# Kernel tuning notes

Measured on AMD Instinct MI355X. Metric: run time of the kernel, lower is better.

## Reference

```python
import jax, jax.numpy as jnp
import numpy as np

B, N, C, K = 32, 1024, 14, 9      # graphs, residues/graph, atom channels, kNN
E, H, NC = 128, 128, 25           # embed_size, hidden_size, num_classes
NG = 128                          # gaussians in time embedding (== embed_size)


def _ffn(x, W1, b1, W2, b2):
    # nn.Sequential(SiLU, Linear, SiLU, Linear)
    h = jax.nn.silu(x) @ W1 + b1
    return jax.nn.silu(h) @ W2 + b2


def _time_emb(t, Wt1, bt1, Wt2, bt2):
    # GaussianSmearing(0,1,NG) -> Linear -> ReLU -> Linear
    offset = jnp.linspace(0.0, 1.0, NG)
    coeff = -0.5 / (offset[1] - offset[0]) ** 2
    d = t[..., None] - offset + 1e-6
    g = jnp.exp(coeff * d * d)
    return jax.nn.relu(g @ Wt1 + bt1) @ Wt2 + bt2


def _forward(S, X, t, emb, Wt1, bt1, Wt2, bt2, We1, be1, We2, be2,
             Wx1, bx1, Wx2, bx2, Wh1, bh1, Wh2, bh2,
             Wd1, bd1, Wd2, bd2, Wp1, bp1, Wr1, br1, Wr2, br2):
    H0 = emb[S]                                           # [B,N,E]
    Hh = H0 + _time_emb(t, Wt1, bt1, Wt2, bt2)            # H_0 + time_emb
    # dynamic kNN graph on CA coordinates (channel 1), per graph
    ca = X[:, :, 1]                                       # [B,N,3]
    d2 = jnp.sum((ca[:, :, None] - ca[:, None]) ** 2, -1) # [B,N,N]
    d2 = d2 + jnp.eye(N, dtype=d2.dtype) * 1e10           # no self loops
    _, idx = jax.lax.top_k(-d2, K)                        # [B,N,K] neighbor ids
    gather = jax.vmap(lambda a, i: a[i])                  # per-graph gather
    Xnb = gather(X, idx)                                  # [B,N,K,C,3]
    Hnb = gather(Hh, idx)                                 # [B,N,K,E]
    rel = X[:, :, None] - Xnb                             # [B,N,K,C,3]
    # multi-channel radial features (EGNN-style channel Gram matrix)
    radial = jnp.einsum('bnkcd,bnked->bnkce', rel, rel).reshape(B, N, K, C * C) / C
    Hi = jnp.broadcast_to(Hh[:, :, None], (B, N, K, E))
    m = _ffn(jnp.concatenate([Hi, Hnb, radial], -1), We1, be1, We2, be2)  # [B,N,K,H]
    # EGNN coordinate update
    w = _ffn(m, Wx1, bx1, Wx2, bx2)                       # [B,N,K,1]
    X_out = X + jnp.mean(rel * w[..., None], axis=2)      # [B,N,C,3]
    # node update
    Hn = Hh + _ffn(jnp.concatenate([Hh, jnp.sum(m, 2)], -1), Wh1, bh1, Wh2, bh2)
    # symmetric edge-distance FFN: f([src,dst]) + f([dst,src])
    Hs = jnp.broadcast_to(Hn[:, :, None], (B, N, K, E))
    Hd = gather(Hn, idx)
    pd = (_ffn(jnp.concatenate([Hs, Hd], -1), Wd1, bd1, Wd2, bd2)
          + _ffn(jnp.concatenate([Hd, Hs], -1), Wd1, bd1, Wd2, bd2))[..., 0]  # [B,N,K]
    # pred_logits = ffn_residue2(pre_H_0 * sigmoid(ffn_proj(H)))
    gate = jax.nn.sigmoid(jax.nn.silu(Hn) @ Wp1 + bp1)
    logits = _ffn(H0 * gate, Wr1, br1, Wr2, br2)          # [B,N,NC]
    return logits, X_out, pd


def setup_inputs() -> dict:
    key = jax.random.key(0)
    ks = jax.random.split(key, 34)
    p = lambda k, s: (0.02 * jax.random.normal(k, s)).astype(jnp.float32)
    inp = {
        'X': jax.random.normal(ks[0], (B, N, C, 3), jnp.float32),
        'S': jax.random.randint(ks[1], (B, N), 0, NC),
        't': jax.random.uniform(ks[2], (B, N), jnp.float32),
        'emb': p(ks[3], (NC, E)),
        'Wt1': p(ks[4], (NG, H)), 'bt1': jnp.zeros((H,), jnp.float32),
        'Wt2': p(ks[5], (H, E)), 'bt2': jnp.zeros((E,), jnp.float32),
        'We1': p(ks[6], (2 * E + C * C, H)), 'be1': jnp.zeros((H,), jnp.float32),
        'We2': p(ks[7], (H, H)), 'be2': jnp.zeros((H,), jnp.float32),
        'Wx1': p(ks[8], (H, H)), 'bx1': jnp.zeros((H,), jnp.float32),
        'Wx2': p(ks[9], (H, 1)), 'bx2': jnp.zeros((1,), jnp.float32),
        'Wh1': p(ks[10], (E + H, H)), 'bh1': jnp.zeros((H,), jnp.float32),
        'Wh2': p(ks[11], (H, E)), 'bh2': jnp.zeros((E,), jnp.float32),
        'Wd1': p(ks[12], (2 * E, H)), 'bd1': jnp.zeros((H,), jnp.float32),
        'Wd2': p(ks[13], (H, 1)), 'bd2': jnp.zeros((1,), jnp.float32),
        'Wp1': p(ks[14], (E, E)), 'bp1': jnp.zeros((E,), jnp.float32),
        'Wr1': p(ks[15], (E, H)), 'br1': jnp.zeros((H,), jnp.float32),
        'Wr2': p(ks[16], (H, NC)), 'br2': jnp.zeros((NC,), jnp.float32),
    }
    return inp


def reference(X, S, t, emb, Wt1, bt1, Wt2, bt2, We1, be1, We2, be2,
              Wx1, bx1, Wx2, bx2, Wh1, bh1, Wh2, bh2,
              Wd1, bd1, Wd2, bd2, Wp1, bp1, Wr1, br1, Wr2, br2):
    return _forward(S, X, t, emb, Wt1, bt1, Wt2, bt2, We1, be1, We2, be2,
                    Wx1, bx1, Wx2, bx2, Wh1, bh1, Wh2, bh2,
                    Wd1, bd1, Wd2, bd2, Wp1, bp1, Wr1, br1, Wr2, br2)
```

## Files before the change

### kernel.cpp

```cpp
#include <hip/hip_runtime.h>

#define BATCH 32
#define NPT   1024
#define CC    14
#define KNN   9
#define EDIM  128
#define HDIM  128
#define NCLS  25
#define BN    (BATCH*NPT)

#define RSTR  236
#define SSTR  140

typedef float  v4f __attribute__((ext_vector_type(4)));
typedef __bf16 v8bf __attribute__((ext_vector_type(8)));

__device__ __forceinline__ float silu_f(float x) {
    const float e = __expf(-x);
    return x * __builtin_amdgcn_rcpf(1.0f + e);
}
__device__ __forceinline__ float sigm_f(float x) {
    const float e = __expf(-x);
    return __builtin_amdgcn_rcpf(1.0f + e);
}
// ... 34 lines not shown
    i -= 16384;
    if (i < 32768) { const int c = i/256, k = i%256; Wh1t[i] = f2bf_rne(Wh1[(size_t)k*128 + c]); return; }
    i -= 32768;
    if (i < 16384) { Wh2t[i] = f2bf_rne(Wh2[(size_t)(i % 128)*128 + i/128]); return; }
    i -= 16384;
    if (i < 32768) {
        const int t = i/128, k = i%128;
        Wd1t[i] = f2bf_rne((t < 128) ? Wd1[(size_t)k*128 + t] : Wd1[(size_t)(128 + k)*128 + (t - 128)]);
        return;
    }
    i -= 32768;
    if (i < 16384) { Wp1t[i] = f2bf_rne(Wp1[(size_t)(i % 128)*128 + i/128]); return; }
    i -= 16384;
    if (i < 16384) { Wr1t[i] = f2bf_rne(Wr1[(size_t)(i % 128)*128 + i/128]); return; }
    i -= 16384;
    if (i < 16384) { Wt1t[i] = f2bf_rne(Wt1[(size_t)(i % 128)*128 + i/128]); return; }
    i -= 16384;
    if (i < 16384) { Wt2t[i] = f2bf_rne(Wt2[(size_t)(i % 128)*128 + i/128]); return; }
    i -= 16384;
    if (i < 32768) {
        const int t = i/128, k = i%128;
        We1Ft[i] = f2bf_rne((t < 128) ? We1[(size_t)k*128 + t] : We1[(size_t)(128 + k)*128 + (t - 128)]);
    }
}

__global__ __launch_bounds__(256) void k_hhP(
    const float* __restrict__ t, const int* __restrict__ S,
    const float* __restrict__ emb,
    const unsigned short* __restrict__ Wt1t, const float* __restrict__ bt1,
    const unsigned short* __restrict__ Wt2t, const float* __restrict__ bt2,
    const unsigned short* __restrict__ We1Ft, const float* __restrict__ be1,
    float* __restrict__ Hh, float* __restrict__ P)
{
    __shared__ __align__(16) unsigned short A0[16*140];
    __shared__ __align__(16) unsigned short A1[16*140];
    __shared__ __align__(16) unsigned short A2[16*140];
    __shared__ int sInt[16];

    const int tid  = threadIdx.x;
    const int wv   = tid >> 6, lane = tid & 63;
    const int quad = lane >> 4, r16 = lane & 15;
    const int col  = tid & 127, rh = tid >> 7;
    const int base = blockIdx.x * 16;

    if (tid < 16) sInt[tid] = S[base + tid];

    const float step  = 1.0f / 127.0f;
    const float coeff = -0.5f / (step * step);
    const float off   = step * (float)col;
    #pragma unroll
    for (int rr = 0; rr < 8; ++rr) {
        const int r = rh*8 + rr;
        const float d = t[base + r] - off + 1e-6f;
        A0[r*140 + col] = f2bf(__expf(coeff * d * d));
    }
    __syncthreads();

    {
        v8bf a[4];
        #pragma unroll
        for (int ks = 0; ks < 4; ++ks)
            a[ks] = *(const v8bf*)(A0 + r16*140 + ks*32 + quad*8);
        #pragma unroll
        for (int c2 = 0; c2 < 2; ++c2) {
            const int ch = (wv*2 + c2)*16 + r16;
            v4f acc = (v4f){0,0,0,0};
            #pragma unroll
            for (int ks = 0; ks < 4; ++ks) {
                const v8bf bb = *(const v8bf*)(Wt1t + (size_t)ch*128 + ks*32 + quad*8);
                acc = __builtin_amdgcn_mfma_f32_16x16x32_bf16(a[ks], bb, acc, 0, 0, 0);
            }
            const float bc = bt1[ch];
            #pragma unroll
            for (int rr = 0; rr < 4; ++rr)
                A1[(quad*4 + rr)*140 + ch] = f2bf(fmaxf(acc[rr] + bc, 0.0f));
        }
    }
    __syncthreads();

    {
        v8bf a[4];
        #pragma unroll
        for (int ks = 0; ks < 4; ++ks)
            a[ks] = *(const v8bf*)(A1 + r16*140 + ks*32 + quad*8);
        #pragma unroll
        for (int c2 = 0; c2 < 2; ++c2) {
            const int ch = (wv*2 + c2)*16 + r16;
            v4f acc = (v4f){0,0,0,0};
            #pragma unroll
            for (int ks = 0; ks < 4; ++ks) {
                const v8bf bb = *(const v8bf*)(Wt2t + (size_t)ch*128 + ks*32 + quad*8);
                acc = __builtin_amdgcn_mfma_f32_16x16x32_bf16(a[ks], bb, acc, 0, 0, 0);
            }
            const float bc = bt2[ch];
            #pragma unroll
            for (int rr = 0; rr < 4; ++rr) {
                const int row = quad*4 + rr;
                const int node = base + row;
                const float hh = emb[sInt[row]*128 + ch] + acc[rr] + bc;
                Hh[(size_t)node*128 + ch] = hh;
                A2[row*140 + ch] = f2bf(silu_f(hh));
            }
        }
    }
    __syncthreads();

    {
        v8bf a[4];
        #pragma unroll
        for (int ks = 0; ks < 4; ++ks)
            a[ks] = *(const v8bf*)(A2 + r16*140 + ks*32 + quad*8);
        #pragma unroll
        for (int c2 = 0; c2 < 4; ++c2) {
            const int ch = (wv*4 + c2)*16 + r16;
            v4f acc = (v4f){0,0,0,0};
            #pragma unroll
            for (int ks = 0; ks < 4; ++ks) {
                const v8bf bb = *(const v8bf*)(We1Ft + (size_t)ch*128 + ks*32 + quad*8);
                acc = __builtin_amdgcn_mfma_f32_16x16x32_bf16(a[ks], bb, acc, 0, 0, 0);
            }
            const float fb = (ch < 128) ? be1[ch] : 0.0f;
            #pragma unroll
            for (int rr = 0; rr < 4; ++rr)
                P[(size_t)(base + quad*4 + rr)*256 + ch] = acc[rr] + fb;
        }
    }
}

__global__ __launch_bounds__(256) void k_knn(
    const float* __restrict__ X, int* __restrict__ idxb)
{
    __shared__ __align__(16) float4 Cc[NPT];
    __shared__ float dsh[4][64][KNN];
    __shared__ int   ish[4][64][KNN];

    const int tid = threadIdx.x, lane = tid & 63, wv = tid >> 6;
    const int bb = blockIdx.x >> 4;
    const int n0 = (blockIdx.x & 15) << 6;
    const float* Xb = X + (size_t)bb * NPT * 42;

    for (int i = tid; i < NPT; i += 256) {
        const float* p = Xb + (size_t)i*42 + 3;
        Cc[i] = make_float4(p[0], p[1], p[2], 0.0f);
    }
    __syncthreads();

    const int n = n0 + lane;
    const float4 c = Cc[n];

    float dist[KNN]; int ind[KNN];
    #pragma unroll
    for (int k = 0; k < KNN; ++k) { dist[k] = 3.0e38f; ind[k] = -1; }

    const int j0 = wv * 256;
    for (int jj = 0; jj < 256; ++jj) {
        const int j = j0 + jj;
        const float4 q = Cc[j];
// ... 24 lines not shown
        for (int w = 0; w < 4; ++w)
            #pragma unroll
            for (int k = 0; k < KNN; ++k) {
                const float d = dsh[w][tid][k];
                const int   i = ish[w][tid][k];
                if (d < fd[KNN-1]) {
                    fd[KNN-1] = d; fi[KNN-1] = i;
                    #pragma unroll
                    for (int p = KNN-1; p > 0; --p) {
                        if (fd[p] < fd[p-1]) {
                            float td = fd[p]; fd[p] = fd[p-1]; fd[p-1] = td;
                            int   ti = fi[p]; fi[p] = fi[p-1]; fi[p-1] = ti;
                        }
                    }
                }
            }
        const int node = (bb << 10) + n0 + tid;
        #pragma unroll
        for (int k = 0; k < KNN; ++k) idxb[(size_t)node*KNN + k] = fi[k];
    }
}

__global__ __launch_bounds__(256) void k_edge(
    const float* __restrict__ X, const int* __restrict__ idxb,
    const float* __restrict__ P,
    const unsigned short* __restrict__ WeRt,
    const unsigned short* __restrict__ We2t,
    const unsigned short* __restrict__ Wx1t,
    const float* __restrict__ be2,
    const float* __restrict__ bx1, const float* __restrict__ Wx2,
    const float* __restrict__ bx2,
    float* __restrict__ msum, float* __restrict__ wbuf)
{
    __shared__ unsigned short radF[16*RSTR];
    __shared__ unsigned short silA[16*SSTR];
    __shared__ unsigned short silB[16*SSTR];
    __shared__ __align__(16) float relS[16][57];
    __shared__ __align__(16) float xS[16][57];
    __shared__ float wred[KNN][16][4];
    __shared__ int   jsh[16][12];

    const int tid  = threadIdx.x;
    const int wv   = tid >> 6, lane = tid & 63;
    const int quad = lane >> 4, r16 = lane & 15;
    const int node0 = blockIdx.x * 16;
    const int b     = node0 >> 10;
    const int chan0 = (wv*2 + 0)*16 + r16;
    const int chan1 = (wv*2 + 1)*16 + r16;
    const int srow  = tid >> 4, c16 = tid & 15;

    if (tid < 144) jsh[tid/9][tid%9] = idxb[(size_t)(node0 + tid/9)*KNN + tid%9];
    {
        const int i0 = c16*3;
        if (i0 < 42) {
            #pragma unroll
            for (int k = 0; k < 3; ++k)
                xS[srow][c16*4 + k] = X[(size_t)(node0 + srow)*42 + i0 + k];
        }
    }

    float pn0[4], pn1[4];
    #pragma unroll
    for (int rr = 0; rr < 4; ++rr) {
        pn0[rr] = P[(size_t)(node0 + quad*4 + rr)*256 + chan0];
        pn1[rr] = P[(size_t)(node0 + quad*4 + rr)*256 + chan1];
    }
    const float be2c0 = be2[chan0], be2c1 = be2[chan1];
    const float bxc0  = bx1[chan0], bxc1  = bx1[chan1];
    const float wxc0  = Wx2[chan0], wxc1  = Wx2[chan1];

    v8bf B1[2][7], B2[2][4], B3[2][4];
    #pragma unroll
    for (int c2 = 0; c2 < 2; ++c2) {
        const int ct = wv*2 + c2;
        #pragma unroll
        for (int ks = 0; ks < 7; ++ks)
            B1[c2][ks] = *(const v8bf*)(WeRt + (size_t)(ct*16 + r16)*224 + ks*32 + quad*8);
        #pragma unroll
        for (int ks = 0; ks < 4; ++ks) {
            B2[c2][ks] = *(const v8bf*)(We2t + (size_t)(ct*16 + r16)*128 + ks*32 + quad*8);
            B3[c2][ks] = *(const v8bf*)(Wx1t + (size_t)(ct*16 + r16)*128 + ks*32 + quad*8);
        }
    }

    float msA0[4] = {0,0,0,0}, msA1[4] = {0,0,0,0};

    __syncthreads();

    for (int t = 0; t < KNN; ++t) {
        {
            const int j  = jsh[srow][t];
            const int i0 = c16*3;
            if (i0 < 42) {
                const size_t jb = (size_t)((b << 10) + j)*42;
                #pragma unroll
                for (int k = 0; k < 3; ++k)
                    relS[srow][c16*4 + k] = xS[srow][c16*4 + k] - X[jb + i0 + k];
            }
        }
        __syncthreads();

        {
            const float* rb = relS[srow];
            #pragma unroll
            for (int kk = 0; kk < 14; ++kk) {
                const int f = c16 + 16*kk;
                if (f < 196) {
                    const int cI = f / 14, eI = f % 14;
                    const float v = (rb[cI*4]*rb[eI*4] + rb[cI*4+1]*rb[eI*4+1]
                                   + rb[cI*4+2]*rb[eI*4+2]) * (1.0f/14.0f);
                    radF[srow*RSTR + f] = f2bf(silu_f(v));
                } else {
                    radF[srow*RSTR + f] = 0;
                }
            }
        }
        __syncthreads();

        v4f acc10 = (v4f){0,0,0,0}, acc11 = (v4f){0,0,0,0};
        #pragma unroll
        for (int ks = 0; ks < 7; ++ks) {
            const v8bf a = *(const v8bf*)(radF + r16*RSTR + ks*32 + quad*8);
            acc10 = __builtin_amdgcn_mfma_f32_16x16x32_bf16(a, B1[0][ks], acc10, 0, 0, 0);
            acc11 = __builtin_amdgcn_mfma_f32_16x16x32_bf16(a, B1[1][ks], acc11, 0, 0, 0);
        }
        {
            float pj0[4], pj1[4];
            #pragma unroll
            for (int rr = 0; rr < 4; ++rr) {
                const int jq = jsh[quad*4 + rr][t];
                const size_t jrow = (size_t)((b << 10) + jq)*256 + 128;
                pj0[rr] = P[jrow + chan0];
                pj1[rr] = P[jrow + chan1];
            }
            #pragma unroll
            for (int rr = 0; rr < 4; ++rr) {
                const int rw = quad*4 + rr;
                silA[rw*SSTR + chan0] = f2bf(silu_f(acc10[rr] + pn0[rr] + pj0[rr]));
                silA[rw*SSTR + chan1] = f2bf(silu_f(acc11[rr] + pn1[rr] + pj1[rr]));
            }
        }
        __syncthreads();

        v4f acc20 = (v4f){0,0,0,0}, acc21 = (v4f){0,0,0,0};
        #pragma unroll
        for (int ks = 0; ks < 4; ++ks) {
            const v8bf a = *(const v8bf*)(silA + r16*SSTR + ks*32 + quad*8);
            acc20 = __builtin_amdgcn_mfma_f32_16x16x32_bf16(a, B2[0][ks], acc20, 0, 0, 0);
            acc21 = __builtin_amdgcn_mfma_f32_16x16x32_bf16(a, B2[1][ks], acc21, 0, 0, 0);
        }
        #pragma unroll
        for (int rr = 0; rr < 4; ++rr) {
            const float m0 = acc20[rr] + be2c0;
            const float m1 = acc21[rr] + be2c1;
            msA0[rr] += m0;  msA1[rr] += m1;
            const int rw = quad*4 + rr;
            silB[rw*SSTR + chan0] = f2bf(silu_f(m0));
            silB[rw*SSTR + chan1] = f2bf(silu_f(m1));
        }
        __syncthreads();

        v4f acc30 = (v4f){0,0,0,0}, acc31 = (v4f){0,0,0,0};
        #pragma unroll
        for (int ks = 0; ks < 4; ++ks) {
            const v8bf a = *(const v8bf*)(silB + r16*SSTR + ks*32 + quad*8);
            acc30 = __builtin_amdgcn_mfma_f32_16x16x32_bf16(a, B3[0][ks], acc30, 0, 0, 0);
            acc31 = __builtin_amdgcn_mfma_f32_16x16x32_bf16(a, B3[1][ks], acc31, 0, 0, 0);
        }
        #pragma unroll
        for (int rr = 0; rr < 4; ++rr) {
            float pr = silu_f(acc30[rr] + bxc0) * wxc0
                     + silu_f(acc31[rr] + bxc1) * wxc1;
            pr += __shfl_xor(pr, 1);
            pr += __shfl_xor(pr, 2);
            pr += __shfl_xor(pr, 4);
            pr += __shfl_xor(pr, 8);
            if (r16 == 0) wred[t][quad*4 + rr][wv] = pr;
        }
    }

    #pragma unroll
    for (int rr = 0; rr < 4; ++rr) {
        msum[(size_t)(node0 + quad*4 + rr)*128 + chan0] = msA0[rr];
        msum[(size_t)(node0 + quad*4 + rr)*128 + chan1] = msA1[rr];
    }
    __syncthreads();
    if (tid < 16*KNN) {
        const int tt = tid / 16, rw = tid % 16;
        wbuf[(size_t)(node0 + rw)*KNN + tt] =
            wred[tt][rw][0] + wred[tt][rw][1] + wred[tt][rw][2] + wred[tt][rw][3] + bx2[0];
    }
}

__global__ __launch_bounds__(256) void k_nodeF(
    const float* __restrict__ X, const float* __restrict__ Hh,
    const float* __restrict__ msum, const int* __restrict__ idxb,
    const float* __restrict__ wbuf,
    const unsigned short* __restrict__ Wh1t, const float* __restrict__ bh1,
    const unsigned short* __restrict__ Wh2t, const float* __restrict__ bh2,
    const unsigned short* __restrict__ Wd1t, const float* __restrict__ bd1,
    const int* __restrict__ S, const float* __restrict__ emb,
    const unsigned short* __restrict__ Wp1t, const float* __restrict__ bp1,
    const unsigned short* __restrict__ Wr1t, const float* __restrict__ br1,
    const float* __restrict__ Wr2, const float* __restrict__ br2,
    float* __restrict__ Hn, float* __restrict__ AB,
    float* __restrict__ outL, float* __restrict__ outX)
{
    __shared__ __align__(16) unsigned short A0[16*268];
    __shared__ __align__(16) unsigned short A1[16*140];
    __shared__ __align__(16) unsigned short A2[16*140];
    __shared__ __align__(16) unsigned short A3[16*140];
    __shared__ int sInt[16];
    float* A4 = (float*)A0;

    const int tid  = threadIdx.x;
    const int wv   = tid >> 6, lane = tid & 63;
    const int quad = lane >> 4, r16 = lane & 15;
    const int base = blockIdx.x * 16;

    if (tid < 16) sInt[tid] = S[base + tid];
    for (int r = 0; r < 16; ++r) {
        const int node = base + r;
        const float v = (tid < 128) ? Hh[(size_t)node*128 + tid]
                                    : msum[(size_t)node*128 + (tid - 128)];
        A0[r*268 + tid] = f2bf(silu_f(v));
    }
    __syncthreads();

    {
        v8bf a[8];
        #pragma unroll
        for (int ks = 0; ks < 8; ++ks)
            a[ks] = *(const v8bf*)(A0 + r16*268 + ks*32 + quad*8);
        #pragma unroll
        for (int c2 = 0; c2 < 2; ++c2) {
            const int ch = (wv*2 + c2)*16 + r16;
            v4f acc = (v4f){0,0,0,0};
            #pragma unroll
            for (int ks = 0; ks < 8; ++ks) {
                const v8bf bb = *(const v8bf*)(Wh1t + (size_t)ch*256 + ks*32 + quad*8);
                acc = __builtin_amdgcn_mfma_f32_16x16x32_bf16(a[ks], bb, acc, 0, 0, 0);
            }
            const float bc = bh1[ch];
            #pragma unroll
            for (int rr = 0; rr < 4; ++rr)
                A1[(quad*4 + rr)*140 + ch] = f2bf(silu_f(acc[rr] + bc));
        }
    }
    __syncthreads();

    {
        v8bf a[4];
        #pragma unroll
        for (int ks = 0; ks < 4; ++ks)
            a[ks] = *(const v8bf*)(A1 + r16*140 + ks*32 + quad*8);
        #pragma unroll
        for (int c2 = 0; c2 < 2; ++c2) {
            const int ch = (wv*2 + c2)*16 + r16;
            v4f acc = (v4f){0,0,0,0};
            #pragma unroll
            for (int ks = 0; ks < 4; ++ks) {
                const v8bf bb = *(const v8bf*)(Wh2t + (size_t)ch*128 + ks*32 + quad*8);
                acc = __builtin_amdgcn_mfma_f32_16x16x32_bf16(a[ks], bb, acc, 0, 0, 0);
            }
            const float bc = bh2[ch];
            #pragma unroll
            for (int rr = 0; rr < 4; ++rr) {
                const int row = quad*4 + rr;
                const int node = base + row;
                const float hn = Hh[(size_t)node*128 + ch] + acc[rr] + bc;
                Hn[(size_t)node*128 + ch] = hn;
                A2[row*140 + ch] = f2bf(silu_f(hn));
            }
        }
    }
    __syncthreads();

    {
        v8bf a[4];
        #pragma unroll
        for (int ks = 0; ks < 4; ++ks)
            a[ks] = *(const v8bf*)(A2 + r16*140 + ks*32 + quad*8);

        #pragma unroll
        for (int cg = 0; cg < 2; ++cg) {
            #pragma unroll
            for (int c2 = 0; c2 < 2; ++c2) {
                const int ch = (wv*4 + cg*2 + c2)*16 + r16;
                v4f acc = (v4f){0,0,0,0};
                #pragma unroll
                for (int ks = 0; ks < 4; ++ks) {
                    const v8bf bb = *(const v8bf*)(Wd1t + (size_t)ch*128 + ks*32 + quad*8);
                    acc = __builtin_amdgcn_mfma_f32_16x16x32_bf16(a[ks], bb, acc, 0, 0, 0);
                }
                const float fb = (ch < 128) ? bd1[ch] : 0.0f;
                #pragma unroll
                for (int rr = 0; rr < 4; ++rr)
                    AB[(size_t)(base + quad*4 + rr)*256 + ch] = acc[rr] + fb;
            }
        }

        #pragma unroll
        for (int c2 = 0; c2 < 2; ++c2) {
            const int ch = (wv*2 + c2)*16 + r16;
            v4f acc = (v4f){0,0,0,0};
            #pragma unroll
            for (int ks = 0; ks < 4; ++ks) {
                const v8bf bb = *(const v8bf*)(Wp1t + (size_t)ch*128 + ks*32 + quad*8);
                acc = __builtin_amdgcn_mfma_f32_16x16x32_bf16(a[ks], bb, acc, 0, 0, 0);
            }
            const float bc = bp1[ch];
            #pragma unroll
            for (int rr = 0; rr < 4; ++rr) {
                const int row = quad*4 + rr;
                const float g = sigm_f(acc[rr] + bc);
                const float x = emb[sInt[row]*128 + ch] * g;
                A3[row*140 + ch] = f2bf(silu_f(x));
            }
        }
    }
    __syncthreads();

    {
        v8bf a[4];
        #pragma unroll
        for (int ks = 0; ks < 4; ++ks)
            a[ks] = *(const v8bf*)(A3 + r16*140 + ks*32 + quad*8);
        #pragma unroll
        for (int c2 = 0; c2 < 2; ++c2) {
            const int ch = (wv*2 + c2)*16 + r16;
            v4f acc = (v4f){0,0,0,0};
            #pragma unroll
            for (int ks = 0; ks < 4; ++ks) {
                const v8bf bb = *(const v8bf*)(Wr1t + (size_t)ch*128 + ks*32 + quad*8);
                acc = __builtin_amdgcn_mfma_f32_16x16x32_bf16(a[ks], bb, acc, 0, 0, 0);
            }
            const float bc = br1[ch];
            #pragma unroll
            for (int rr = 0; rr < 4; ++rr)
                A4[(quad*4 + rr)*134 + ch] = silu_f(acc[rr] + bc);
        }
    }
    __syncthreads();

    for (int o = tid; o < 16*NCLS; o += 256) {
        const int r = o / NCLS, j = o % NCLS;
        float s = 0.0f;
        for (int i = 0; i < 128; ++i) s += A4[r*134 + i] * Wr2[i*NCLS + j];
        outL[(size_t)(base + r)*NCLS + j] = s + br2[j];
    }

    for (int o = tid; o < 16*CC*3; o += 256) {
        const int r = o / (CC*3), q = o % (CC*3);
        const int node = base + r;
        const int bq = node >> 10;
        const int cq = q / 3, dc = q % 3;
        const float xv = X[((size_t)node*CC + cq)*3 + dc];
        float a = 0.0f;
        for (int k = 0; k < KNN; ++k) {
            const int j = idxb[(size_t)node*KNN + k];
            const float xj = X[(((size_t)(bq << 10) + j)*CC + cq)*3 + dc];
            a += (xv - xj) * wbuf[(size_t)node*KNN + k];
        }
        outX[(size_t)node*CC*3 + q] = xv + a / 9.0f;
    }
}

__global__ __launch_bounds__(256) void k_pd2(
    const float* __restrict__ AB, const int* __restrict__ idxb,
    const float* __restrict__ Wd2, const float* __restrict__ bd2,
    float* __restrict__ outPd)
{
    const int tid  = threadIdx.x;
    const int lane = tid & 63, wv = tid >> 6;
    const int c0   = lane, c1 = lane + 64;
    const float w0 = Wd2[c0], w1 = Wd2[c1];
    const float b2 = 2.0f * bd2[0];

    #pragma unroll
    for (int s = 0; s < 2; ++s) {
        const int node = blockIdx.x * 8 + wv*2 + s;
        const int b    = node >> 10;

        int jv = 0;
        if (lane < KNN) jv = idxb[(size_t)node*KNN + lane];

        const float An0 = AB[(size_t)node*256 + c0];
        const float An1 = AB[(size_t)node*256 + c1];
        const float Bn0 = AB[(size_t)node*256 + 128 + c0];
        const float Bn1 = AB[(size_t)node*256 + 128 + c1];

        float Aj0[KNN], Aj1[KNN], Bj0[KNN], Bj1[KNN];
        #pragma unroll
        for (int e = 0; e < KNN; ++e) {
            const size_t jn = (size_t)((b << 10) + __shfl(jv, e)) * 256;
// ... 42 lines not shown
    const float* Wp1 = (const float*)d_in[24];
    const float* bp1 = (const float*)d_in[25];
    const float* Wr1 = (const float*)d_in[26];
    const float* br1 = (const float*)d_in[27];
    const float* Wr2 = (const float*)d_in[28];
    const float* br2 = (const float*)d_in[29];

    float* out   = (float*)d_out;
    float* outL  = out;
    float* outX  = out + (size_t)BN*NCLS;
    float* outPd = outX + (size_t)BN*CC*3;

    unsigned short* WeRt  = (unsigned short*)d_ws;
    unsigned short* We2t  = WeRt  + 28672;
    unsigned short* Wx1t  = We2t  + 16384;
    unsigned short* Wh1t  = Wx1t  + 16384;
    unsigned short* Wh2t  = Wh1t  + 32768;
    unsigned short* Wd1t  = Wh2t  + 16384;
    unsigned short* Wp1t  = Wd1t  + 32768;
    unsigned short* Wr1t  = Wp1t  + 16384;
    unsigned short* Wt1t  = Wr1t  + 16384;
    unsigned short* Wt2t  = Wt1t  + 16384;
    unsigned short* We1Ft = Wt2t  + 16384;
    float* Hh   = (float*)(We1Ft + 32768);
    float* msum = Hh   + (size_t)BN*EDIM;
    float* Hn   = msum + (size_t)BN*HDIM;
    float* wbuf = Hn   + (size_t)BN*EDIM;
    float* P    = wbuf + (size_t)BN*KNN;
    int*   idxb = (int*)(P + (size_t)BN*256);

    k_prep  <<<944,    256, 0, stream>>>(We1, We2, Wx1, Wh1, Wh2, Wd1, Wp1, Wr1, Wt1, Wt2,
                                         WeRt, We2t, Wx1t, Wh1t, Wh2t, Wd1t, Wp1t, Wr1t,
                                         Wt1t, Wt2t, We1Ft);
    k_hhP   <<<BN/16,  256, 0, stream>>>(t, S, emb, Wt1t, bt1, Wt2t, bt2, We1Ft, be1, Hh, P);
    k_knn   <<<BN/64,  256, 0, stream>>>(X, idxb);
    k_edge  <<<BN/16,  256, 0, stream>>>(X, idxb, P, WeRt, We2t, Wx1t,
                                         be2, bx1, Wx2, bx2, msum, wbuf);
    k_nodeF <<<BN/16,  256, 0, stream>>>(X, Hh, msum, idxb, wbuf,
                                         Wh1t, bh1, Wh2t, bh2, Wd1t, bd1,
                                         S, emb, Wp1t, bp1, Wr1t, br1, Wr2, br2,
                                         Hn, P, outL, outX);
    k_pd2   <<<BN/8,   256, 0, stream>>>(P, idxb, Wd2, bd2, outPd);
}
```

Baseline: 503.9 us.

## Process 32 nodes per block so each weight fragment feeds two MFMA row groups

```diff
diff --git a/kernel.cpp b/kernel.cpp
--- a/kernel.cpp
+++ b/kernel.cpp
@@ -90,97 +90,112 @@
     const unsigned short* __restrict__ We1Ft, const float* __restrict__ be1,
     float* __restrict__ Hh, float* __restrict__ P)
 {
-    __shared__ __align__(16) unsigned short A0[16*140];
-    __shared__ __align__(16) unsigned short A1[16*140];
-    __shared__ __align__(16) unsigned short A2[16*140];
-    __shared__ int sInt[16];
+    __shared__ __align__(16) unsigned short A0[32*140];
+    __shared__ __align__(16) unsigned short A1[32*140];
+    __shared__ __align__(16) unsigned short A2[32*140];
+    __shared__ int sInt[32];
 
     const int tid  = threadIdx.x;
     const int wv   = tid >> 6, lane = tid & 63;
     const int quad = lane >> 4, r16 = lane & 15;
     const int col  = tid & 127, rh = tid >> 7;
-    const int base = blockIdx.x * 16;
-
-    if (tid < 16) sInt[tid] = S[base + tid];
+    const int base = blockIdx.x * 32;
+
+    if (tid < 32) sInt[tid] = S[base + tid];
 
     const float step  = 1.0f / 127.0f;
     const float coeff = -0.5f / (step * step);
     const float off   = step * (float)col;
     #pragma unroll
-    for (int rr = 0; rr < 8; ++rr) {
-        const int r = rh*8 + rr;
+    for (int rr = 0; rr < 16; ++rr) {
+        const int r = rh*16 + rr;
         const float d = t[base + r] - off + 1e-6f;
         A0[r*140 + col] = f2bf(__expf(coeff * d * d));
     }
     __syncthreads();
 
     {
-        v8bf a[4];
-        #pragma unroll
-        for (int ks = 0; ks < 4; ++ks)
-            a[ks] = *(const v8bf*)(A0 + r16*140 + ks*32 + quad*8);
+        v8bf a[2][4];
+        #pragma unroll
+        for (int g = 0; g < 2; ++g)
+            #pragma unroll
+            for (int ks = 0; ks < 4; ++ks)
+                a[g][ks] = *(const v8bf*)(A0 + (16*g + r16)*140 + ks*32 + quad*8);
         #pragma unroll
         for (int c2 = 0; c2 < 2; ++c2) {
             const int ch = (wv*2 + c2)*16 + r16;
-            v4f acc = (v4f){0,0,0,0};
+            v4f acc[2] = {(v4f){0,0,0,0}, (v4f){0,0,0,0}};
             #pragma unroll
             for (int ks = 0; ks < 4; ++ks) {
                 const v8bf bb = *(const v8bf*)(Wt1t + (size_t)ch*128 + ks*32 + quad*8);
-                acc = __builtin_amdgcn_mfma_f32_16x16x32_bf16(a[ks], bb, acc, 0, 0, 0);
+                acc[0] = __builtin_amdgcn_mfma_f32_16x16x32_bf16(a[0][ks], bb, acc[0], 0, 0, 0);
+                acc[1] = __builtin_amdgcn_mfma_f32_16x16x32_bf16(a[1][ks], bb, acc[1], 0, 0, 0);
             }
             const float bc = bt1[ch];
             #pragma unroll
-            for (int rr = 0; rr < 4; ++rr)
-                A1[(quad*4 + rr)*140 + ch] = f2bf(fmaxf(acc[rr] + bc, 0.0f));
+            for (int g = 0; g < 2; ++g)
+                #pragma unroll
+                for (int rr = 0; rr < 4; ++rr)
+                    A1[(16*g + quad*4 + rr)*140 + ch] = f2bf(fmaxf(acc[g][rr] + bc, 0.0f));
         }
     }
     __syncthreads();
 
     {
-        v8bf a[4];
-        #pragma unroll
-        for (int ks = 0; ks < 4; ++ks)
-            a[ks] = *(const v8bf*)(A1 + r16*140 + ks*32 + quad*8);
+        v8bf a[2][4];
+        #pragma unroll
+        for (int g = 0; g < 2; ++g)
+            #pragma unroll
+            for (int ks = 0; ks < 4; ++ks)
+                a[g][ks] = *(const v8bf*)(A1 + (16*g + r16)*140 + ks*32 + quad*8);
         #pragma unroll
         for (int c2 = 0; c2 < 2; ++c2) {
             const int ch = (wv*2 + c2)*16 + r16;
-            v4f acc = (v4f){0,0,0,0};
+            v4f acc[2] = {(v4f){0,0,0,0}, (v4f){0,0,0,0}};
             #pragma unroll
             for (int ks = 0; ks < 4; ++ks) {
                 const v8bf bb = *(const v8bf*)(Wt2t + (size_t)ch*128 + ks*32 + quad*8);
-                acc = __builtin_amdgcn_mfma_f32_16x16x32_bf16(a[ks], bb, acc, 0, 0, 0);
+                acc[0] = __builtin_amdgcn_mfma_f32_16x16x32_bf16(a[0][ks], bb, acc[0], 0, 0, 0);
+                acc[1] = __builtin_amdgcn_mfma_f32_16x16x32_bf16(a[1][ks], bb, acc[1], 0, 0, 0);
             }
             const float bc = bt2[ch];
             #pragma unroll
-            for (int rr = 0; rr < 4; ++rr) {
-                const int row = quad*4 + rr;
-                const int node = base + row;
-                const float hh = emb[sInt[row]*128 + ch] + acc[rr] + bc;
-                Hh[(size_t)node*128 + ch] = hh;
-                A2[row*140 + ch] = f2bf(silu_f(hh));
-            }
+            for (int g = 0; g < 2; ++g)
+                #pragma unroll
+                for (int rr = 0; rr < 4; ++rr) {
+                    const int row = 16*g + quad*4 + rr;
+                    const int node = base + row;
+                    const float hh = emb[sInt[row]*128 + ch] + acc[g][rr] + bc;
+                    Hh[(size_t)node*128 + ch] = hh;
+                    A2[row*140 + ch] = f2bf(silu_f(hh));
+                }
         }
     }
     __syncthreads();
 
     {
-        v8bf a[4];
-        #pragma unroll
-        for (int ks = 0; ks < 4; ++ks)
-            a[ks] = *(const v8bf*)(A2 + r16*140 + ks*32 + quad*8);
+        v8bf a[2][4];
+        #pragma unroll
+        for (int g = 0; g < 2; ++g)
+            #pragma unroll
+            for (int ks = 0; ks < 4; ++ks)
+                a[g][ks] = *(const v8bf*)(A2 + (16*g + r16)*140 + ks*32 + quad*8);
         #pragma unroll
         for (int c2 = 0; c2 < 4; ++c2) {
             const int ch = (wv*4 + c2)*16 + r16;
-            v4f acc = (v4f){0,0,0,0};
+            v4f acc[2] = {(v4f){0,0,0,0}, (v4f){0,0,0,0}};
             #pragma unroll
             for (int ks = 0; ks < 4; ++ks) {
                 const v8bf bb = *(const v8bf*)(We1Ft + (size_t)ch*128 + ks*32 + quad*8);
-                acc = __builtin_amdgcn_mfma_f32_16x16x32_bf16(a[ks], bb, acc, 0, 0, 0);
+                acc[0] = __builtin_amdgcn_mfma_f32_16x16x32_bf16(a[0][ks], bb, acc[0], 0, 0, 0);
+                acc[1] = __builtin_amdgcn_mfma_f32_16x16x32_bf16(a[1][ks], bb, acc[1], 0, 0, 0);
             }
             const float fb = (ch < 128) ? be1[ch] : 0.0f;
             #pragma unroll
-            for (int rr = 0; rr < 4; ++rr)
-                P[(size_t)(base + quad*4 + rr)*256 + ch] = acc[rr] + fb;
+            for (int g = 0; g < 2; ++g)
+                #pragma unroll
+                for (int rr = 0; rr < 4; ++rr)
+                    P[(size_t)(base + 16*g + quad*4 + rr)*256 + ch] = acc[g][rr] + fb;
         }
     }
 }
@@ -271,76 +286,103 @@
     const float* __restrict__ bx2,
     float* __restrict__ msum, float* __restrict__ wbuf)
 {
-    __shared__ unsigned short radF[16*RSTR];
-    __shared__ unsigned short silA[16*SSTR];
-    __shared__ unsigned short silB[16*SSTR];
-    __shared__ __align__(16) float relS[16][57];
-    __shared__ __align__(16) float xS[16][57];
-    __shared__ float wred[KNN][16][4];
-    __shared__ int   jsh[16][12];
+    __shared__ unsigned short radF[32*RSTR];
+    __shared__ __align__(16) unsigned char UA[32*SSTR*2];
+    __shared__ unsigned short silB[32*SSTR];
+    __shared__ float wred[KNN][32][4];
+    __shared__ int   jsh[32][KNN];
+
+    unsigned short* silA = (unsigned short*)UA;
+    float*          relS = (float*)UA;
 
     const int tid  = threadIdx.x;
     const int wv   = tid >> 6, lane = tid & 63;
     const int quad = lane >> 4, r16 = lane & 15;
-    const int node0 = blockIdx.x * 16;
+    const int node0 = blockIdx.x * 32;
     const int b     = node0 >> 10;
     const int chan0 = (wv*2 + 0)*16 + r16;
     const int chan1 = (wv*2 + 1)*16 + r16;
     const int srow  = tid >> 4, c16 = tid & 15;
 
-    if (tid < 144) jsh[tid/9][tid%9] = idxb[(size_t)(node0 + tid/9)*KNN + tid%9];
-    {
-        const int i0 = c16*3;
-        if (i0 < 42) {
+    for (int o = tid; o < 32*KNN; o += 256)
+        jsh[o/KNN][o%KNN] = idxb[(size_t)(node0 + o/KNN)*KNN + o%KNN];
+
+    float xr[2][3] = {{0,0,0},{0,0,0}};
+    if (c16 < 14) {
+        #pragma unroll
+        for (int g = 0; g < 2; ++g)
             #pragma unroll
             for (int k = 0; k < 3; ++k)
-                xS[srow][c16*4 + k] = X[(size_t)(node0 + srow)*42 + i0 + k];
-        }
-    }
-
-    float pn0[4], pn1[4];
+                xr[g][k] = X[(size_t)(node0 + srow + 16*g)*42 + c16*3 + k];
+    }
+
+    float pn0[2][4], pn1[2][4];
     #pragma unroll
-    for (int rr = 0; rr < 4; ++rr) {
-        pn0[rr] = P[(size_t)(node0 + quad*4 + rr)*256 + chan0];
-        pn1[rr] = P[(size_t)(node0 + quad*4 + rr)*256 + chan1];
-    }
+    for (int g = 0; g < 2; ++g)
+        #pragma unroll
+        for (int rr = 0; rr < 4; ++rr) {
+            const size_t nrow = (size_t)(node0 + 16*g + quad*4 + rr)*256;
+            pn0[g][rr] = P[nrow + chan0];
+            pn1[g][rr] = P[nrow + chan1];
+        }
     const float be2c0 = be2[chan0], be2c1 = be2[chan1];
     const float bxc0  = bx1[chan0], bxc1  = bx1[chan1];
     const float wxc0  = Wx2[chan0], wxc1  = Wx2[chan1];
 
-    v8bf B1[2][7], B2[2][4], B3[2][4];
-    #pragma unroll
-    for (int c2 = 0; c2 < 2; ++c2) {
-        const int ct = wv*2 + c2;
-        #pragma unroll
-        for (int ks = 0; ks < 7; ++ks)
-            B1[c2][ks] = *(const v8bf*)(WeRt + (size_t)(ct*16 + r16)*224 + ks*32 + quad*8);
-        #pragma unroll
-        for (int ks = 0; ks < 4; ++ks) {
-            B2[c2][ks] = *(const v8bf*)(We2t + (size_t)(ct*16 + r16)*128 + ks*32 + quad*8);
-            B3[c2][ks] = *(const v8bf*)(Wx1t + (size_t)(ct*16 + r16)*128 + ks*32 + quad*8);
-        }
-    }
-
-    float msA0[4] = {0,0,0,0}, msA1[4] = {0,0,0,0};
-
-    __syncthreads();
+    float msA0[2][4] = {{0,0,0,0},{0,0,0,0}};
+    float msA1[2][4] = {{0,0,0,0},{0,0,0,0}};
+
+    __syncthreads();
+
+    float xj[2][3];
+    if (c16 < 14) {
+        #pragma unroll
+        for (int g = 0; g < 2; ++g) {
+            const int j = jsh[srow + 16*g][0];
+            #pragma unroll
+            for (int k = 0; k < 3; ++k)
+                xj[g][k] = X[(size_t)((b << 10) + j)*42 + c16*3 + k];
+        }
+    }
 
     for (int t = 0; t < KNN; ++t) {
-        {
-            const int j  = jsh[srow][t];
-            const int i0 = c16*3;
-            if (i0 < 42) {
-                const size_t jb = (size_t)((b << 10) + j)*42;
+        if (c16 < 14) {
+            #pragma unroll
+            for (int g = 0; g < 2; ++g)
                 #pragma unroll
                 for (int k = 0; k < 3; ++k)
-                    relS[srow][c16*4 + k] = xS[srow][c16*4 + k] - X[jb + i0 + k];
-            }
-        }
-        __syncthreads();
-
-        {
-            const float* rb = relS[srow];
+                    relS[(srow + 16*g)*70 + c16*4 + k] = xr[g][k] - xj[g][k];
+        }
+        if (t + 1 < KNN && c16 < 14) {
+            #pragma unroll
+            for (int g = 0; g < 2; ++g) {
+                const int j = jsh[srow + 16*g][t+1];
+                #pragma unroll
+                for (int k = 0; k < 3; ++k)
+                    xj[g][k] = X[(size_t)((b << 10) + j)*42 + c16*3 + k];
+            }
+        }
+        float pj0[2][4], pj1[2][4];
+        #pragma unroll
+        for (int g = 0; g < 2; ++g)
+            #pragma unroll
+            for (int rr = 0; rr < 4; ++rr) {
+                const int jq = jsh[16*g + quad*4 + rr][t];
+                const size_t jrow = (size_t)((b << 10) + jq)*256 + 128;
+                pj0[g][rr] = P[jrow + chan0];
+                pj1[g][rr] = P[jrow + chan1];
+            }
+        v8bf B1c0[7], B1c1[7];
+        #pragma unroll
+        for (int ks = 0; ks < 7; ++ks) {
+            B1c0[ks] = *(const v8bf*)(WeRt + (size_t)chan0*224 + ks*32 + quad*8);
+            B1c1[ks] = *(const v8bf*)(WeRt + (size_t)chan1*224 + ks*32 + quad*8);
+        }
+
+        #pragma unroll
+        for (int g = 0; g < 2; ++g) {
+            const int row = srow + 16*g;
+            const float* rb = relS + row*70;
             #pragma unroll
             for (int kk = 0; kk < 14; ++kk) {
                 const int f = c16 + 16*kk;
@@ -348,84 +390,103 @@
                     const int cI = f / 14, eI = f % 14;
                     const float v = (rb[cI*4]*rb[eI*4] + rb[cI*4+1]*rb[eI*4+1]
                                    + rb[cI*4+2]*rb[eI*4+2]) * (1.0f/14.0f);
-                    radF[srow*RSTR + f] = f2bf(silu_f(v));
+                    radF[row*RSTR + f] = f2bf(silu_f(v));
                 } else {
-                    radF[srow*RSTR + f] = 0;
+                    radF[row*RSTR + f] = 0;
                 }
             }
         }
         __syncthreads();
 
-        v4f acc10 = (v4f){0,0,0,0}, acc11 = (v4f){0,0,0,0};
-        #pragma unroll
-        for (int ks = 0; ks < 7; ++ks) {
-            const v8bf a = *(const v8bf*)(radF + r16*RSTR + ks*32 + quad*8);
-            acc10 = __builtin_amdgcn_mfma_f32_16x16x32_bf16(a, B1[0][ks], acc10, 0, 0, 0);
-            acc11 = __builtin_amdgcn_mfma_f32_16x16x32_bf16(a, B1[1][ks], acc11, 0, 0, 0);
-        }
-        {
-            float pj0[4], pj1[4];
+        v4f a10[2] = {(v4f){0,0,0,0},(v4f){0,0,0,0}};
+        v4f a11[2] = {(v4f){0,0,0,0},(v4f){0,0,0,0}};
+        #pragma unroll
+        for (int g = 0; g < 2; ++g)
+            #pragma unroll
+            for (int ks = 0; ks < 7; ++ks) {
+                const v8bf a = *(const v8bf*)(radF + (16*g + r16)*RSTR + ks*32 + quad*8);
+                a10[g] = __builtin_amdgcn_mfma_f32_16x16x32_bf16(a, B1c0[ks], a10[g], 0, 0, 0);
+                a11[g] = __builtin_amdgcn_mfma_f32_16x16x32_bf16(a, B1c1[ks], a11[g], 0, 0, 0);
+            }
+        v8bf B2c0[4], B2c1[4];
+        #pragma unroll
+        for (int ks = 0; ks < 4; ++ks) {
+            B2c0[ks] = *(const v8bf*)(We2t + (size_t)chan0*128 + ks*32 + quad*8);
+            B2c1[ks] = *(const v8bf*)(We2t + (size_t)chan1*128 + ks*32 + quad*8);
+        }
+        #pragma unroll
+        for (int g = 0; g < 2; ++g)
             #pragma unroll
             for (int rr = 0; rr < 4; ++rr) {
-                const int jq = jsh[quad*4 + rr][t];
-                const size_t jrow = (size_t)((b << 10) + jq)*256 + 128;
-                pj0[rr] = P[jrow + chan0];
-                pj1[rr] = P[jrow + chan1];
-            }
+                const int rw = 16*g + quad*4 + rr;
+                silA[rw*SSTR + chan0] = f2bf(silu_f(a10[g][rr] + pn0[g][rr] + pj0[g][rr]));
+                silA[rw*SSTR + chan1] = f2bf(silu_f(a11[g][rr] + pn1[g][rr] + pj1[g][rr]));
+            }
+        __syncthreads();
+
+        v4f a20[2] = {(v4f){0,0,0,0},(v4f){0,0,0,0}};
+        v4f a21[2] = {(v4f){0,0,0,0},(v4f){0,0,0,0}};
+        #pragma unroll
+        for (int g = 0; g < 2; ++g)
+            #pragma unroll
+            for (int ks = 0; ks < 4; ++ks) {
+                const v8bf a = *(const v8bf*)(silA + (16*g + r16)*SSTR + ks*32 + quad*8);
+                a20[g] = __builtin_amdgcn_mfma_f32_16x16x32_bf16(a, B2c0[ks], a20[g], 0, 0, 0);
+                a21[g] = __builtin_amdgcn_mfma_f32_16x16x32_bf16(a, B2c1[ks], a21[g], 0, 0, 0);
+            }
+        v8bf B3c0[4], B3c1[4];
+        #pragma unroll
+        for (int ks = 0; ks < 4; ++ks) {
+            B3c0[ks] = *(const v8bf*)(Wx1t + (size_t)chan0*128 + ks*32 + quad*8);
+            B3c1[ks] = *(const v8bf*)(Wx1t + (size_t)chan1*128 + ks*32 + quad*8);
+        }
+        #pragma unroll
+        for (int g = 0; g < 2; ++g)
             #pragma unroll
             for (int rr = 0; rr < 4; ++rr) {
-                const int rw = quad*4 + rr;
-                silA[rw*SSTR + chan0] = f2bf(silu_f(acc10[rr] + pn0[rr] + pj0[rr]));
-                silA[rw*SSTR + chan1] = f2bf(silu_f(acc11[rr] + pn1[rr] + pj1[rr]));
-            }
-        }
+                const float m0 = a20[g][rr] + be2c0;
+                const float m1 = a21[g][rr] + be2c1;
+                msA0[g][rr] += m0;  msA1[g][rr] += m1;
+                const int rw = 16*g + quad*4 + rr;
+                silB[rw*SSTR + chan0] = f2bf(silu_f(m0));
+                silB[rw*SSTR + chan1] = f2bf(silu_f(m1));
+            }
         __syncthreads();
 
-        v4f acc20 = (v4f){0,0,0,0}, acc21 = (v4f){0,0,0,0};
-        #pragma unroll
-        for (int ks = 0; ks < 4; ++ks) {
-            const v8bf a = *(const v8bf*)(silA + r16*SSTR + ks*32 + quad*8);
-            acc20 = __builtin_amdgcn_mfma_f32_16x16x32_bf16(a, B2[0][ks], acc20, 0, 0, 0);
-            acc21 = __builtin_amdgcn_mfma_f32_16x16x32_bf16(a, B2[1][ks], acc21, 0, 0, 0);
-        }
+        v4f a30[2] = {(v4f){0,0,0,0},(v4f){0,0,0,0}};
+        v4f a31[2] = {(v4f){0,0,0,0},(v4f){0,0,0,0}};
+        #pragma unroll
+        for (int g = 0; g < 2; ++g)
+            #pragma unroll
+            for (int ks = 0; ks < 4; ++ks) {
+                const v8bf a = *(const v8bf*)(silB + (16*g + r16)*SSTR + ks*32 + quad*8);
+                a30[g] = __builtin_amdgcn_mfma_f32_16x16x32_bf16(a, B3c0[ks], a30[g], 0, 0, 0);
+                a31[g] = __builtin_amdgcn_mfma_f32_16x16x32_bf16(a, B3c1[ks], a31[g], 0, 0, 0);
+            }
+        #pragma unroll
+        for (int g = 0; g < 2; ++g)
+            #pragma unroll
+            for (int rr = 0; rr < 4; ++rr) {
+                float pr = silu_f(a30[g][rr] + bxc0) * wxc0
+                         + silu_f(a31[g][rr] + bxc1) * wxc1;
+                pr += __shfl_xor(pr, 1);
+                pr += __shfl_xor(pr, 2);
+                pr += __shfl_xor(pr, 4);
+                pr += __shfl_xor(pr, 8);
+                if (r16 == 0) wred[t][16*g + quad*4 + rr][wv] = pr;
+            }
+    }
+
+    #pragma unroll
+    for (int g = 0; g < 2; ++g)
         #pragma unroll
         for (int rr = 0; rr < 4; ++rr) {
-            const float m0 = acc20[rr] + be2c0;
-            const float m1 = acc21[rr] + be2c1;
-            msA0[rr] += m0;  msA1[rr] += m1;
-            const int rw = quad*4 + rr;
-            silB[rw*SSTR + chan0] = f2bf(silu_f(m0));
-            silB[rw*SSTR + chan1] = f2bf(silu_f(m1));
-        }
-        __syncthreads();
-
-        v4f acc30 = (v4f){0,0,0,0}, acc31 = (v4f){0,0,0,0};
-        #pragma unroll
-        for (int ks = 0; ks < 4; ++ks) {
-            const v8bf a = *(const v8bf*)(silB + r16*SSTR + ks*32 + quad*8);
-            acc30 = __builtin_amdgcn_mfma_f32_16x16x32_bf16(a, B3[0][ks], acc30, 0, 0, 0);
-            acc31 = __builtin_amdgcn_mfma_f32_16x16x32_bf16(a, B3[1][ks], acc31, 0, 0, 0);
-        }
-        #pragma unroll
-        for (int rr = 0; rr < 4; ++rr) {
-            float pr = silu_f(acc30[rr] + bxc0) * wxc0
-                     + silu_f(acc31[rr] + bxc1) * wxc1;
-            pr += __shfl_xor(pr, 1);
-            pr += __shfl_xor(pr, 2);
-            pr += __shfl_xor(pr, 4);
-            pr += __shfl_xor(pr, 8);
-            if (r16 == 0) wred[t][quad*4 + rr][wv] = pr;
-        }
-    }
-
-    #pragma unroll
-    for (int rr = 0; rr < 4; ++rr) {
-        msum[(size_t)(node0 + quad*4 + rr)*128 + chan0] = msA0[rr];
-        msum[(size_t)(node0 + quad*4 + rr)*128 + chan1] = msA1[rr];
-    }
-    __syncthreads();
-    if (tid < 16*KNN) {
-        const int tt = tid / 16, rw = tid % 16;
+            msum[(size_t)(node0 + 16*g + quad*4 + rr)*128 + chan0] = msA0[g][rr];
+            msum[(size_t)(node0 + 16*g + quad*4 + rr)*128 + chan1] = msA1[g][rr];
+        }
+    __syncthreads();
+    for (int o = tid; o < 32*KNN; o += 256) {
+        const int tt = o / 32, rw = o % 32;
         wbuf[(size_t)(node0 + rw)*KNN + tt] =
             wred[tt][rw][0] + wred[tt][rw][1] + wred[tt][rw][2] + wred[tt][rw][3] + bx2[0];
     }
@@ -445,20 +506,20 @@
     float* __restrict__ Hn, float* __restrict__ AB,
     float* __restrict__ outL, float* __restrict__ outX)
 {
-    __shared__ __align__(16) unsigned short A0[16*268];
-    __shared__ __align__(16) unsigned short A1[16*140];
-    __shared__ __align__(16) unsigned short A2[16*140];
-    __shared__ __align__(16) unsigned short A3[16*140];
-    __shared__ int sInt[16];
+    __shared__ __align__(16) unsigned short A0[32*268];
+    __shared__ __align__(16) unsigned short A1[32*140];
+    __shared__ __align__(16) unsigned short A2[32*140];
+    __shared__ __align__(16) unsigned short A3[32*140];
+    __shared__ int sInt[32];
     float* A4 = (float*)A0;
 
     const int tid  = threadIdx.x;
     const int wv   = tid >> 6, lane = tid & 63;
     const int quad = lane >> 4, r16 = lane & 15;
-    const int base = blockIdx.x * 16;
-
-    if (tid < 16) sInt[tid] = S[base + tid];
-    for (int r = 0; r < 16; ++r) {
+    const int base = blockIdx.x * 32;
+
+    if (tid < 32) sInt[tid] = S[base + tid];
+    for (int r = 0; r < 32; ++r) {
         const int node = base + r;
         const float v = (tid < 128) ? Hh[(size_t)node*128 + tid]
                                     : msum[(size_t)node*128 + (tid - 128)];
@@ -467,129 +528,149 @@
     __syncthreads();
 
     {
-        v8bf a[8];
-        #pragma unroll
-        for (int ks = 0; ks < 8; ++ks)
-            a[ks] = *(const v8bf*)(A0 + r16*268 + ks*32 + quad*8);
+        v8bf a[2][8];
+        #pragma unroll
+        for (int g = 0; g < 2; ++g)
+            #pragma unroll
+            for (int ks = 0; ks < 8; ++ks)
+                a[g][ks] = *(const v8bf*)(A0 + (16*g + r16)*268 + ks*32 + quad*8);
         #pragma unroll
         for (int c2 = 0; c2 < 2; ++c2) {
             const int ch = (wv*2 + c2)*16 + r16;
-            v4f acc = (v4f){0,0,0,0};
+            v4f acc[2] = {(v4f){0,0,0,0}, (v4f){0,0,0,0}};
             #pragma unroll
             for (int ks = 0; ks < 8; ++ks) {
                 const v8bf bb = *(const v8bf*)(Wh1t + (size_t)ch*256 + ks*32 + quad*8);
-                acc = __builtin_amdgcn_mfma_f32_16x16x32_bf16(a[ks], bb, acc, 0, 0, 0);
+                acc[0] = __builtin_amdgcn_mfma_f32_16x16x32_bf16(a[0][ks], bb, acc[0], 0, 0, 0);
+                acc[1] = __builtin_amdgcn_mfma_f32_16x16x32_bf16(a[1][ks], bb, acc[1], 0, 0, 0);
             }
             const float bc = bh1[ch];
             #pragma unroll
-            for (int rr = 0; rr < 4; ++rr)
-                A1[(quad*4 + rr)*140 + ch] = f2bf(silu_f(acc[rr] + bc));
+            for (int g = 0; g < 2; ++g)
+                #pragma unroll
+                for (int rr = 0; rr < 4; ++rr)
+                    A1[(16*g + quad*4 + rr)*140 + ch] = f2bf(silu_f(acc[g][rr] + bc));
         }
     }
     __syncthreads();
 
     {
-        v8bf a[4];
-        #pragma unroll
-        for (int ks = 0; ks < 4; ++ks)
-            a[ks] = *(const v8bf*)(A1 + r16*140 + ks*32 + quad*8);
+        v8bf a[2][4];
+        #pragma unroll
+        for (int g = 0; g < 2; ++g)
+            #pragma unroll
+            for (int ks = 0; ks < 4; ++ks)
+                a[g][ks] = *(const v8bf*)(A1 + (16*g + r16)*140 + ks*32 + quad*8);
         #pragma unroll
         for (int c2 = 0; c2 < 2; ++c2) {
             const int ch = (wv*2 + c2)*16 + r16;
-            v4f acc = (v4f){0,0,0,0};
+            v4f acc[2] = {(v4f){0,0,0,0}, (v4f){0,0,0,0}};
             #pragma unroll
             for (int ks = 0; ks < 4; ++ks) {
                 const v8bf bb = *(const v8bf*)(Wh2t + (size_t)ch*128 + ks*32 + quad*8);
-                acc = __builtin_amdgcn_mfma_f32_16x16x32_bf16(a[ks], bb, acc, 0, 0, 0);
+                acc[0] = __builtin_amdgcn_mfma_f32_16x16x32_bf16(a[0][ks], bb, acc[0], 0, 0, 0);
+                acc[1] = __builtin_amdgcn_mfma_f32_16x16x32_bf16(a[1][ks], bb, acc[1], 0, 0, 0);
             }
             const float bc = bh2[ch];
             #pragma unroll
-            for (int rr = 0; rr < 4; ++rr) {
-                const int row = quad*4 + rr;
-                const int node = base + row;
-                const float hn = Hh[(size_t)node*128 + ch] + acc[rr] + bc;
-                Hn[(size_t)node*128 + ch] = hn;
-                A2[row*140 + ch] = f2bf(silu_f(hn));
-            }
+            for (int g = 0; g < 2; ++g)
+                #pragma unroll
+                for (int rr = 0; rr < 4; ++rr) {
+                    const int row = 16*g + quad*4 + rr;
+                    const int node = base + row;
+                    const float hn = Hh[(size_t)node*128 + ch] + acc[g][rr] + bc;
+                    Hn[(size_t)node*128 + ch] = hn;
+                    A2[row*140 + ch] = f2bf(silu_f(hn));
+                }
         }
     }
     __syncthreads();
 
     {
-        v8bf a[4];
-        #pragma unroll
-        for (int ks = 0; ks < 4; ++ks)
-            a[ks] = *(const v8bf*)(A2 + r16*140 + ks*32 + quad*8);
-
-        #pragma unroll
-        for (int cg = 0; cg < 2; ++cg) {
-            #pragma unroll
-            for (int c2 = 0; c2 < 2; ++c2) {
-                const int ch = (wv*4 + cg*2 + c2)*16 + r16;
-                v4f acc = (v4f){0,0,0,0};
-                #pragma unroll
-                for (int ks = 0; ks < 4; ++ks) {
-                    const v8bf bb = *(const v8bf*)(Wd1t + (size_t)ch*128 + ks*32 + quad*8);
-                    acc = __builtin_amdgcn_mfma_f32_16x16x32_bf16(a[ks], bb, acc, 0, 0, 0);
-                }
-                const float fb = (ch < 128) ? bd1[ch] : 0.0f;
+        v8bf a[2][4];
+        #pragma unroll
+        for (int g = 0; g < 2; ++g)
+            #pragma unroll
+            for (int ks = 0; ks < 4; ++ks)
+                a[g][ks] = *(const v8bf*)(A2 + (16*g + r16)*140 + ks*32 + quad*8);
+
+        #pragma unroll
+        for (int c2 = 0; c2 < 4; ++c2) {
+            const int ch = (wv*4 + c2)*16 + r16;
+            v4f acc[2] = {(v4f){0,0,0,0}, (v4f){0,0,0,0}};
+            #pragma unroll
+            for (int ks = 0; ks < 4; ++ks) {
+                const v8bf bb = *(const v8bf*)(Wd1t + (size_t)ch*128 + ks*32 + quad*8);
+                acc[0] = __builtin_amdgcn_mfma_f32_16x16x32_bf16(a[0][ks], bb, acc[0], 0, 0, 0);
+                acc[1] = __builtin_amdgcn_mfma_f32_16x16x32_bf16(a[1][ks], bb, acc[1], 0, 0, 0);
+            }
+            const float fb = (ch < 128) ? bd1[ch] : 0.0f;
+            #pragma unroll
+            for (int g = 0; g < 2; ++g)
                 #pragma unroll
                 for (int rr = 0; rr < 4; ++rr)
-                    AB[(size_t)(base + quad*4 + rr)*256 + ch] = acc[rr] + fb;
-            }
+                    AB[(size_t)(base + 16*g + quad*4 + rr)*256 + ch] = acc[g][rr] + fb;
         }
 
         #pragma unroll
         for (int c2 = 0; c2 < 2; ++c2) {
             const int ch = (wv*2 + c2)*16 + r16;
-            v4f acc = (v4f){0,0,0,0};
+            v4f acc[2] = {(v4f){0,0,0,0}, (v4f){0,0,0,0}};
             #pragma unroll
             for (int ks = 0; ks < 4; ++ks) {
                 const v8bf bb = *(const v8bf*)(Wp1t + (size_t)ch*128 + ks*32 + quad*8);
-                acc = __builtin_amdgcn_mfma_f32_16x16x32_bf16(a[ks], bb, acc, 0, 0, 0);
+                acc[0] = __builtin_amdgcn_mfma_f32_16x16x32_bf16(a[0][ks], bb, acc[0], 0, 0, 0);
+                acc[1] = __builtin_amdgcn_mfma_f32_16x16x32_bf16(a[1][ks], bb, acc[1], 0, 0, 0);
             }
             const float bc = bp1[ch];
             #pragma unroll
-            for (int rr = 0; rr < 4; ++rr) {
-                const int row = quad*4 + rr;
-                const float g = sigm_f(acc[rr] + bc);
-                const float x = emb[sInt[row]*128 + ch] * g;
-                A3[row*140 + ch] = f2bf(silu_f(x));
-            }
+            for (int g = 0; g < 2; ++g)
+                #pragma unroll
+                for (int rr = 0; rr < 4; ++rr) {
+                    const int row = 16*g + quad*4 + rr;
+                    const float gg = sigm_f(acc[g][rr] + bc);
+                    const float x = emb[sInt[row]*128 + ch] * gg;
+                    A3[row*140 + ch] = f2bf(silu_f(x));
+                }
         }
     }
     __syncthreads();
 
     {
-        v8bf a[4];
-        #pragma unroll
-        for (int ks = 0; ks < 4; ++ks)
-            a[ks] = *(const v8bf*)(A3 + r16*140 + ks*32 + quad*8);
+        v8bf a[2][4];
+        #pragma unroll
+        for (int g = 0; g < 2; ++g)
+            #pragma unroll
+            for (int ks = 0; ks < 4; ++ks)
+                a[g][ks] = *(const v8bf*)(A3 + (16*g + r16)*140 + ks*32 + quad*8);
         #pragma unroll
         for (int c2 = 0; c2 < 2; ++c2) {
             const int ch = (wv*2 + c2)*16 + r16;
-            v4f acc = (v4f){0,0,0,0};
+            v4f acc[2] = {(v4f){0,0,0,0}, (v4f){0,0,0,0}};
             #pragma unroll
             for (int ks = 0; ks < 4; ++ks) {
                 const v8bf bb = *(const v8bf*)(Wr1t + (size_t)ch*128 + ks*32 + quad*8);
-                acc = __builtin_amdgcn_mfma_f32_16x16x32_bf16(a[ks], bb, acc, 0, 0, 0);
+                acc[0] = __builtin_amdgcn_mfma_f32_16x16x32_bf16(a[0][ks], bb, acc[0], 0, 0, 0);
+                acc[1] = __builtin_amdgcn_mfma_f32_16x16x32_bf16(a[1][ks], bb, acc[1], 0, 0, 0);
             }
             const float bc = br1[ch];
             #pragma unroll
-            for (int rr = 0; rr < 4; ++rr)
-                A4[(quad*4 + rr)*134 + ch] = silu_f(acc[rr] + bc);
-        }
-    }
-    __syncthreads();
-
-    for (int o = tid; o < 16*NCLS; o += 256) {
+            for (int g = 0; g < 2; ++g)
+                #pragma unroll
+                for (int rr = 0; rr < 4; ++rr)
+                    A4[(16*g + quad*4 + rr)*134 + ch] = silu_f(acc[g][rr] + bc);
+        }
+    }
+    __syncthreads();
+
+    for (int o = tid; o < 32*NCLS; o += 256) {
         const int r = o / NCLS, j = o % NCLS;
         float s = 0.0f;
         for (int i = 0; i < 128; ++i) s += A4[r*134 + i] * Wr2[i*NCLS + j];
         outL[(size_t)(base + r)*NCLS + j] = s + br2[j];
     }
 
-    for (int o = tid; o < 16*CC*3; o += 256) {
+    for (int o = tid; o < 32*CC*3; o += 256) {
         const int r = o / (CC*3), q = o % (CC*3);
         const int node = base + r;
         const int bq = node >> 10;
@@ -598,8 +679,8 @@
         float a = 0.0f;
         for (int k = 0; k < KNN; ++k) {
             const int j = idxb[(size_t)node*KNN + k];
-            const float xj = X[(((size_t)(bq << 10) + j)*CC + cq)*3 + dc];
-            a += (xv - xj) * wbuf[(size_t)node*KNN + k];
+            const float xjv = X[(((size_t)(bq << 10) + j)*CC + cq)*3 + dc];
+            a += (xv - xjv) * wbuf[(size_t)node*KNN + k];
         }
         outX[(size_t)node*CC*3 + q] = xv + a / 9.0f;
     }
@@ -708,11 +789,11 @@
     k_prep  <<<944,    256, 0, stream>>>(We1, We2, Wx1, Wh1, Wh2, Wd1, Wp1, Wr1, Wt1, Wt2,
                                          WeRt, We2t, Wx1t, Wh1t, Wh2t, Wd1t, Wp1t, Wr1t,
                                          Wt1t, Wt2t, We1Ft);
-    k_hhP   <<<BN/16,  256, 0, stream>>>(t, S, emb, Wt1t, bt1, Wt2t, bt2, We1Ft, be1, Hh, P);
+    k_hhP   <<<BN/32,  256, 0, stream>>>(t, S, emb, Wt1t, bt1, Wt2t, bt2, We1Ft, be1, Hh, P);
     k_knn   <<<BN/64,  256, 0, stream>>>(X, idxb);
-    k_edge  <<<BN/16,  256, 0, stream>>>(X, idxb, P, WeRt, We2t, Wx1t,
+    k_edge  <<<BN/32,  256, 0, stream>>>(X, idxb, P, WeRt, We2t, Wx1t,
                                          be2, bx1, Wx2, bx2, msum, wbuf);
-    k_nodeF <<<BN/16,  256, 0, stream>>>(X, Hh, msum, idxb, wbuf,
+    k_nodeF <<<BN/32,  256, 0, stream>>>(X, Hh, msum, idxb, wbuf,
                                          Wh1t, bh1, Wh2t, bh2, Wd1t, bd1,
                                          S, emb, Wp1t, bp1, Wr1t, br1, Wr2, br2,
                                          Hn, P, outL, outX);
```

New measurement: 593.6 us. 17.8% more time.
